# Optimization experiments

Measured on AMD Instinct MI355X. Metric: run time of the kernel, lower is better.

Reference implementation:

```python
import math
import jax, jax.numpy as jnp
import numpy as np

T, B, IN, H, D, ETA, R = 128, 32, 512, 8, 64, 4, 4
DE = ETA * D  # expanded key dim = eta * head_dim
EPS = 1e-05


def setup_inputs() -> dict:
    key = jax.random.key(0)
    ks = jax.random.split(key, 8)
    s = 0.05
    return {
        "inputs": jax.random.normal(ks[0], (T, B, IN), jnp.float32),
        "terminations": jnp.zeros((T, B), jnp.float32),
        "tilde_k_prev": jax.random.normal(ks[1], (B, R, H, DE), jnp.float32) * s,
        "tilde_v_prev": jax.random.normal(ks[2], (B, R, H, D), jnp.float32) * s,
        "s_prev": jax.random.normal(ks[3], (B, H, DE), jnp.float32) * s,
        "tick": jnp.zeros((B, 1), jnp.float32),
        "W_kqv": jax.random.normal(ks[4], (H * D * 5, IN), jnp.float32) * s,
        "b_kqv": jnp.zeros((H * D * 5,), jnp.float32),
        "W_p": jax.random.normal(ks[5], (H * ETA * 3, IN), jnp.float32) * s,
        "b_p": jnp.zeros((H * ETA * 3,), jnp.float32),
        "W_o": jax.random.normal(ks[6], (IN, H * D), jnp.float32) * s,
        "b_o": jnp.zeros((IN,), jnp.float32),
    }


def _forward(inputs, terminations, tilde_k_prev, tilde_v_prev, s_prev, tick,
             W_kqv, b_kqv, W_p, b_p, W_o, b_o):
    # projections
    kqv = (inputs @ W_kqv.T + b_kqv).reshape(T, B, H, 5, D)
    keys, queries, values, beta, gammas = (kqv[..., i, :] for i in range(5))
    p = (inputs @ W_p.T + b_p).reshape(T, B, H, 3, ETA)
    p1, p2, p3 = (p[..., i, :] for i in range(3))
    relu, sig = jax.nn.relu, jax.nn.sigmoid
    # kernel feature maps: outer product then flatten (d outer, n inner)
    keys = jnp.einsum('tbhd,tbhn->tbhdn', relu(keys), relu(p1)).reshape(T, B, H, DE)
    queries = jnp.einsum('tbhd,tbhn->tbhdn', relu(queries), relu(p2)).reshape(T, B, H, DE)
    gammas = jnp.einsum('tbhd,tbhn->tbhdn', sig(gammas), sig(p3)).reshape(T, B, H, DE)
    beta = sig(beta)  # (T,B,H,D)
    # oscillatory basis
    ticks = tick[None] + jnp.arange(1, T + 1, dtype=jnp.float32).reshape(T, 1, 1)  # (T,B,1)
    omegas = jnp.linspace(-math.pi, math.pi, R)
    occil = jnp.cos(ticks * omegas[None, None, :])  # (T,B,R)
    values = values * beta
    values_r = values[:, :, None] * occil[:, :, :, None, None]   # (T,B,R,H,D)
    keys_g = keys * gammas                                        # (T,B,H,DE)
    keys_r = keys_g[:, :, None] * occil[:, :, :, None, None]     # (T,B,R,H,DE)
    # discounts (with termination resets)
    nt = (1.0 - terminations)[:, :, None, None]
    dg = (1.0 - gammas) * nt  # (T,B,H,DE)
    db = (1.0 - beta) * nt    # (T,B,H,D)
    # recurrence y[t] = discount[t]*y[t-1] + x[t] via lax.scan over T
    def step(carry, xs):
        k_st, v_st, s_st = carry
        kx, vx, sx, dgt, dbt = xs
        k_new = dgt[:, None] * k_st + kx   # (B,R,H,DE)
        v_new = dbt[:, None] * v_st + vx   # (B,R,H,D)
        s_new = dgt * s_st + sx            # (B,H,DE)
        return (k_new, v_new, s_new), (k_new, v_new, s_new)
    (kf, vf, sf), (K, V, S) = jax.lax.scan(
        step, (tilde_k_prev, tilde_v_prev, s_prev), (keys_r, values_r, keys_g, dg, db))
    # attention readout
    kdq = jnp.einsum('tbrhd,tbhd->tbrh', K, queries)
    kv = jnp.einsum('tbrhd,tbrh->tbhd', V, kdq)
    norm = jnp.einsum('tbhd,tbhd->tbh', S, queries)
    attn = kv / (2 * R * norm[..., None] + EPS)  # (T,B,H,D)
    out = attn.reshape(T, B, H * D) @ W_o.T + b_o  # dropout p=0 (eval)
    return out, kf, vf, sf, tick + T


def reference(inputs, terminations, tilde_k_prev, tilde_v_prev, s_prev, tick,
              W_kqv, b_kqv, W_p, b_p, W_o, b_o):
    return _forward(inputs, terminations, tilde_k_prev, tilde_v_prev, s_prev, tick,
                    W_kqv, b_kqv, W_p, b_p, W_o, b_o)
```

## Files before the change

kernel.cpp:

```cpp
#include <hip/hip_runtime.h>
#include <math.h>
#include <stdint.h>

constexpr int T_ = 128, B_ = 32, IN_ = 512, H_ = 8, D_ = 64, ETA_ = 4, R_ = 4;
constexpr int DE_ = ETA_ * D_;
constexpr float EPS_ = 1e-5f;
constexpr int M_   = T_ * B_;
constexpr int BH_  = B_ * H_;
constexpr int NC2  = 16;
constexpr int CH2  = T_ / NC2;

constexpr int NW = 2688;
constexpr int SPLITCOL = 1664;

typedef __attribute__((ext_vector_type(8))) short bf16x8;
typedef __attribute__((ext_vector_type(4))) float f32x4;

__device__ __forceinline__ float bf2f(unsigned short u) {
    return __builtin_bit_cast(float, ((unsigned)u) << 16);
}
__device__ __forceinline__ unsigned short f2bf(float f) {
    unsigned u = __builtin_bit_cast(unsigned, f);
    u = (u + 0x7fffu + ((u >> 16) & 1u)) >> 16;
    return (unsigned short)u;
}
__device__ __forceinline__ float fsigm(float x) {
    return __fdividef(1.f, 1.f + __expf(-x));
}

__global__ __launch_bounds__(256) void cast_splitA(
    const float* __restrict__ src, unsigned short* __restrict__ dst, int n4)
{
    int i = blockIdx.x * 256 + threadIdx.x;
    if (i >= n4) return;
    const int r = i >> 7;
    const int c = (i & 127) << 2;
    float4 x = *(const float4*)(src + (size_t)r * 512 + c);
    ushort4 hi = make_ushort4(f2bf(x.x), f2bf(x.y), f2bf(x.z), f2bf(x.w));
    ushort4 lo = make_ushort4(f2bf(x.x - bf2f(hi.x)), f2bf(x.y - bf2f(hi.y)),
                              f2bf(x.z - bf2f(hi.z)), f2bf(x.w - bf2f(hi.w)));
    unsigned short* dr = dst + (size_t)r * 1024 + c;
    *(ushort4*)dr = hi;
    *(ushort4*)(dr + 512) = lo;
}

__global__ __launch_bounds__(256) void build_w2_bias(
    const float* __restrict__ Wkqv, const float* __restrict__ Wp,
    const float* __restrict__ bkqv, const float* __restrict__ bp,
    unsigned short* __restrict__ W2, float* __restrict__ bias_perm)
{
    int i = blockIdx.x * 256 + threadIdx.x;
    if (i >= NW * 128) return;
    const int rr = i >> 7;
    const int c = (i & 127) << 2;

    bool zero = false;
    const float* srow = nullptr;
    float bv = 0.f;
    if (rr < 512) {
        const int h = rr >> 6, dd = rr & 63, s = h * 320 + dd;
        srow = Wkqv + (size_t)s * 512; bv = bkqv[s];
    } else if (rr < 1024) {
        const int q = rr - 512, h = q >> 6, dd = q & 63, s = h * 320 + 64 + dd;
        srow = Wkqv + (size_t)s * 512; bv = bkqv[s];
    } else if (rr < 1536) {
        const int q = rr - 1024, h = q >> 6, dd = q & 63, s = h * 320 + 256 + dd;
        srow = Wkqv + (size_t)s * 512; bv = bkqv[s];
    } else if (rr < 1632) {
        const int q = rr - 1536;
        srow = Wp + (size_t)q * 512; bv = bp[q];
    } else if (rr < 1664) {
        zero = true;
    } else if (rr < 2176) {
        const int q = rr - 1664, h = q >> 6, dd = q & 63, s = h * 320 + 128 + dd;
        srow = Wkqv + (size_t)s * 512; bv = bkqv[s];
    } else {
        const int q = rr - 2176, h = q >> 6, dd = q & 63, s = h * 320 + 192 + dd;
        srow = Wkqv + (size_t)s * 512; bv = bkqv[s];
    }

    float4 x = zero ? make_float4(0.f, 0.f, 0.f, 0.f) : *(const float4*)(srow + c);
    ushort4 hi = make_ushort4(f2bf(x.x), f2bf(x.y), f2bf(x.z), f2bf(x.w));
    ushort4 lo = make_ushort4(f2bf(x.x - bf2f(hi.x)), f2bf(x.y - bf2f(hi.y)),
                              f2bf(x.z - bf2f(hi.z)), f2bf(x.w - bf2f(hi.w)));
    unsigned short* dr = W2 + (size_t)rr * 1536 + c;
    *(ushort4*)dr = hi;
    *(ushort4*)(dr + 512) = lo;
    *(ushort4*)(dr + 1024) = hi;
    if (c == 0) bias_perm[rr] = zero ? 0.f : bv;
}

__global__ __launch_bounds__(256) void cast_f32_bf16(
    const float* __restrict__ src, unsigned short* __restrict__ dst, int n8)
{
    int i = blockIdx.x * 256 + threadIdx.x;
    if (i >= n8) return;
    const float4* s = (const float4*)src;
    float4 a = s[2 * i], b = s[2 * i + 1];
    *(ushort4*)(dst + 8 * i)     = make_ushort4(f2bf(a.x), f2bf(a.y), f2bf(a.z), f2bf(a.w));
    *(ushort4*)(dst + 8 * i + 4) = make_ushort4(f2bf(b.x), f2bf(b.y), f2bf(b.z), f2bf(b.w));
}

__device__ __forceinline__ void gl_lds16(const unsigned short* g, unsigned short* l) {
    __builtin_amdgcn_global_load_lds((const __attribute__((address_space(1))) void*)g,
                                     (__attribute__((address_space(3))) void*)l, 16, 0, 0);
}

template <int BM, int BN>
__global__ __launch_bounds__(256) void gemm_bf16(
    const unsigned short* __restrict__ A,
    const unsigned short* __restrict__ W,
    const float* __restrict__ bias,
    float* __restrict__ C,
    int N, int sA, int sW, int kBig, int kSmall, int splitcol)
{
    constexpr int WM = BM / 2, WN = BN / 2;
    constexpr int AM = WM / 16, AN = WN / 16;
    constexpr int NLA = BM / 64;
    constexpr int NLB = BN / 64;
    constexpr int NLD = NLA + NLB;

    int bx, by;
    {
        const int nwg = gridDim.x * gridDim.y;
        int lin = blockIdx.y * gridDim.x + blockIdx.x;
        lin = (lin & 7) * (nwg >> 3) + (lin >> 3);
        const int G = (gridDim.x % 7 == 0) ? 7 : gridDim.x;
        const int grpsz = gridDim.y * G;
        const int cg = lin / grpsz, rem = lin % grpsz;
        by = rem / G;
        bx = cg * G + rem % G;
    }
    const int bm = by * BM;
    const int bn = bx * BN;
    const int tid = threadIdx.x;
    const int lane = tid & 63;
    const int wid = tid >> 6;
    const int wr = wid >> 1;
    const int wc = wid & 1;

    __shared__ __align__(16) unsigned short As[3][BM * 32];
    __shared__ __align__(16) unsigned short Bs[3][BN * 32];

    const unsigned short* aRow = A + (size_t)(bm + (tid & (BM - 1))) * sA
                                   + (tid / BM) * 8;
    const unsigned short* bRow = W + (size_t)(bn + (tid & (BN - 1))) * sW
                                   + (tid / BN) * 8;

    const int fA = (((lane >> 4) * BM) + wr * WM + (lane & 15)) * 8;
    const int fB = (((lane >> 4) * BN) + wc * WN + (lane & 15)) * 8;

    f32x4 acc[AM][AN] = {};
    const int K = (bn < splitcol) ? kBig : kSmall;
    const int NKT = K >> 5;

    auto stage = [&](int buf, int k0) {
        const int koA = (k0 >= 512) ? k0 - 512 : k0;
#pragma unroll
        for (int i = 0; i < NLA; ++i)
            gl_lds16(aRow + koA + i * (256 / BM) * 8,
                     &As[buf][(i * 256 + wid * 64) * 8]);
#pragma unroll
        for (int i = 0; i < NLB; ++i)
            gl_lds16(bRow + k0 + i * (256 / BN) * 8,
                     &Bs[buf][(i * 256 + wid * 64) * 8]);
    };

    stage(0, 0);
    if (NKT > 1) stage(1, 32);

    for (int kt = 0; kt < NKT; ++kt) {
        const int cur = kt % 3;
        if (kt + 2 < NKT) {
            stage((kt + 2) % 3, (kt + 2) << 5);
            if constexpr (NLD == 4)      asm volatile("s_waitcnt vmcnt(8)\ns_barrier" ::: "memory");
            else if constexpr (NLD == 3) asm volatile("s_waitcnt vmcnt(6)\ns_barrier" ::: "memory");
            else                         asm volatile("s_waitcnt vmcnt(4)\ns_barrier" ::: "memory");
        } else if (kt + 2 == NKT) {
            if constexpr (NLD == 4)      asm volatile("s_waitcnt vmcnt(4)\ns_barrier" ::: "memory");
            else if constexpr (NLD == 3) asm volatile("s_waitcnt vmcnt(3)\ns_barrier" ::: "memory");
            else                         asm volatile("s_waitcnt vmcnt(2)\ns_barrier" ::: "memory");
        } else {
            asm volatile("s_waitcnt vmcnt(0)\ns_barrier" ::: "memory");
        }
        __builtin_amdgcn_sched_barrier(0);

        bf16x8 af[AM], bfr[AN];
#pragma unroll
        for (int m = 0; m < AM; ++m) af[m] = *(const bf16x8*)&As[cur][fA + m * 128];
#pragma unroll
        for (int n = 0; n < AN; ++n) bfr[n] = *(const bf16x8*)&Bs[cur][fB + n * 128];
#pragma unroll
        for (int m = 0; m < AM; ++m)
#pragma unroll
            for (int n = 0; n < AN; ++n)
                acc[m][n] = __builtin_amdgcn_mfma_f32_16x16x32_bf16(af[m], bfr[n], acc[m][n], 0, 0, 0);

        asm volatile("s_waitcnt lgkmcnt(0)\ns_barrier" ::: "memory");
    }

#pragma unroll
    for (int n = 0; n < AN; ++n) {
        const int col = bn + wc * WN + n * 16 + (lane & 15);
        const float bv = bias[col];
#pragma unroll
        for (int m = 0; m < AM; ++m) {
            const int row0 = bm + wr * WM + m * 16 + ((lane >> 4) << 2);
#pragma unroll
            for (int j = 0; j < 4; ++j)
                C[(size_t)(row0 + j) * N + col] = acc[m][n][j] + bv;
        }
    }
}

template <int CTRL, int RM>
__device__ __forceinline__ float dpp_radd(float x) {
    int t = __builtin_amdgcn_update_dpp(0, __builtin_bit_cast(int, x), CTRL, RM, 0xf, true);
    return x + __builtin_bit_cast(float, t);
}
__device__ __forceinline__ float wave_allsum(float x) {
    x = dpp_radd<0x111, 0xf>(x);
    x = dpp_radd<0x112, 0xf>(x);
    x = dpp_radd<0x114, 0xf>(x);
    x = dpp_radd<0x118, 0xf>(x);
    x = dpp_radd<0x142, 0xa>(x);
    x = dpp_radd<0x143, 0xc>(x);
    return __builtin_bit_cast(float, __builtin_amdgcn_readlane(__builtin_bit_cast(int, x), 63));
}

__device__ __forceinline__ void osc2(float tt, float& oc03, float& oc12) {
    oc03 = cosf(3.14159265358979323846f * tt);
    oc12 = cosf(1.04719755119659774615f * tt);
}

__global__ __launch_bounds__(1024) void scan_fused(
    const float* __restrict__ kqv, const float* __restrict__ term,
    const float* __restrict__ tick,
    const float* __restrict__ k_prev, const float* __restrict__ v_prev,
    const float* __restrict__ s_prev,
    unsigned short* __restrict__ attn,
    float* __restrict__ kf, float* __restrict__ vf, float* __restrict__ sf,
    float* __restrict__ tick_out)
{
    const int bh = blockIdx.x;
    const int b = bh >> 3, h = bh & 7;
    const int tid = threadIdx.x;
    const int w = tid >> 6;
    const int d = tid & 63;

    __shared__ float LK[NC2][4][DE_];
    __shared__ float LS[NC2][DE_];
    __shared__ float LV[NC2][4][D_];
    __shared__ float LDg[NC2][DE_];
    __shared__ float LDb[NC2][D_];

    const float tk = tick[b];

    float K0[4] = {}, K1[4] = {}, K2[4] = {}, K3[4] = {}, S[4] = {};
    float V0 = 0.f, V1 = 0.f, V2 = 0.f, V3 = 0.f;
    float Dgv[4] = {1.f, 1.f, 1.f, 1.f};
    float Dbv = 1.f;

    if (w == 0) {
        float4 k4;
        k4 = *(const float4*)&k_prev[((size_t)(b * 4 + 0) * 8 + h) * DE_ + 4 * d];
        K0[0] = k4.x; K0[1] = k4.y; K0[2] = k4.z; K0[3] = k4.w;
        k4 = *(const float4*)&k_prev[((size_t)(b * 4 + 1) * 8 + h) * DE_ + 4 * d];
        K1[0] = k4.x; K1[1] = k4.y; K1[2] = k4.z; K1[3] = k4.w;
        k4 = *(const float4*)&k_prev[((size_t)(b * 4 + 2) * 8 + h) * DE_ + 4 * d];
        K2[0] = k4.x; K2[1] = k4.y; K2[2] = k4.z; K2[3] = k4.w;
        k4 = *(const float4*)&k_prev[((size_t)(b * 4 + 3) * 8 + h) * DE_ + 4 * d];
        K3[0] = k4.x; K3[1] = k4.y; K3[2] = k4.z; K3[3] = k4.w;
        k4 = *(const float4*)&s_prev[((size_t)b * 8 + h) * DE_ + 4 * d];
        S[0] = k4.x; S[1] = k4.y; S[2] = k4.z; S[3] = k4.w;
        V0 = v_prev[((size_t)(b * 4 + 0) * 8 + h) * D_ + d];
        V1 = v_prev[((size_t)(b * 4 + 1) * 8 + h) * D_ + d];
        V2 = v_prev[((size_t)(b * 4 + 2) * 8 + h) * D_ + d];
        V3 = v_prev[((size_t)(b * 4 + 3) * 8 + h) * D_ + d];
    }

    for (int t = w * CH2; t < w * CH2 + CH2; ++t) {
        const float* row = kqv + ((size_t)t * B_ + b) * NW;
        const float c0 = row[h * 64 + d];
        const float c2 = row[1664 + h * 64 + d];
        const float c3 = row[2176 + h * 64 + d];
        const float c4 = row[1024 + h * 64 + d];
        const float* pr = row + 1536 + h * 12;
        const float4 p1 = *(const float4*)pr;
        const float4 p3 = *(const float4*)(pr + 8);
        const float nt = 1.f - term[(size_t)t * B_ + b];

        float oc03, oc12; osc2(tk + (float)(t + 1), oc03, oc12);
        const float sgam = fsigm(c4);
        const float rk = fmaxf(c0, 0.f);
        const float sbet = fsigm(c3);
        const float vb = c2 * sbet;
        const float dbv = (1.f - sbet) * nt;
        const float p1a[4] = {p1.x, p1.y, p1.z, p1.w};
        const float p3a[4] = {p3.x, p3.y, p3.z, p3.w};
#pragma unroll
        for (int n = 0; n < 4; ++n) {
            const float g  = sgam * fsigm(p3a[n]);
            const float kg = rk * fmaxf(p1a[n], 0.f) * g;
            const float dg = (1.f - g) * nt;
            S[n]  = fmaf(dg, S[n],  kg);
            K0[n] = fmaf(dg, K0[n], kg * oc03);
            K1[n] = fmaf(dg, K1[n], kg * oc12);
            K2[n] = fmaf(dg, K2[n], kg * oc12);
            K3[n] = fmaf(dg, K3[n], kg * oc03);
            Dgv[n] *= dg;
        }
        V0 = fmaf(dbv, V0, vb * oc03);
        V1 = fmaf(dbv, V1, vb * oc12);
        V2 = fmaf(dbv, V2, vb * oc12);
        V3 = fmaf(dbv, V3, vb * oc03);
        Dbv *= dbv;
    }

    *(float4*)&LK[w][0][4 * d] = make_float4(K0[0], K0[1], K0[2], K0[3]);
    *(float4*)&LK[w][1][4 * d] = make_float4(K1[0], K1[1], K1[2], K1[3]);
    *(float4*)&LK[w][2][4 * d] = make_float4(K2[0], K2[1], K2[2], K2[3]);
    *(float4*)&LK[w][3][4 * d] = make_float4(K3[0], K3[1], K3[2], K3[3]);
    *(float4*)&LS[w][4 * d]    = make_float4(S[0], S[1], S[2], S[3]);
    LV[w][0][d] = V0; LV[w][1][d] = V1; LV[w][2][d] = V2; LV[w][3][d] = V3;
    *(float4*)&LDg[w][4 * d]   = make_float4(Dgv[0], Dgv[1], Dgv[2], Dgv[3]);
    LDb[w][d] = Dbv;
    __syncthreads();

    if (tid < DE_) {
        const int de = tid;
        float c0 = LK[0][0][de], c1k = LK[0][1][de], c2k = LK[0][2][de],
              c3k = LK[0][3][de], cs = LS[0][de];
        for (int c = 1; c < NC2; ++c) {
            const float dg = LDg[c][de];
            float n0 = fmaf(dg, c0,  LK[c][0][de]); LK[c][0][de] = c0;  c0  = n0;
            float n1 = fmaf(dg, c1k, LK[c][1][de]); LK[c][1][de] = c1k; c1k = n1;
            float n2 = fmaf(dg, c2k, LK[c][2][de]); LK[c][2][de] = c2k; c2k = n2;
            float n3 = fmaf(dg, c3k, LK[c][3][de]); LK[c][3][de] = c3k; c3k = n3;
            float ns = fmaf(dg, cs,  LS[c][de]);    LS[c][de]    = cs;  cs  = ns;
        }
        kf[((size_t)(b * 4 + 0) * 8 + h) * DE_ + de] = c0;
        kf[((size_t)(b * 4 + 1) * 8 + h) * DE_ + de] = c1k;
        kf[((size_t)(b * 4 + 2) * 8 + h) * DE_ + de] = c2k;
        kf[((size_t)(b * 4 + 3) * 8 + h) * DE_ + de] = c3k;
        sf[((size_t)b * 8 + h) * DE_ + de] = cs;
    } else if (tid < DE_ + D_) {
        const int dd = tid - DE_;
        float v0 = LV[0][0][dd], v1 = LV[0][1][dd], v2 = LV[0][2][dd], v3 = LV[0][3][dd];
        for (int c = 1; c < NC2; ++c) {
            const float db = LDb[c][dd];
            float n0 = fmaf(db, v0, LV[c][0][dd]); LV[c][0][dd] = v0; v0 = n0;
            float n1 = fmaf(db, v1, LV[c][1][dd]); LV[c][1][dd] = v1; v1 = n1;
            float n2 = fmaf(db, v2, LV[c][2][dd]); LV[c][2][dd] = v2; v2 = n2;
            float n3 = fmaf(db, v3, LV[c][3][dd]); LV[c][3][dd] = v3; v3 = n3;
        }
        vf[((size_t)(b * 4 + 0) * 8 + h) * D_ + dd] = v0;
        vf[((size_t)(b * 4 + 1) * 8 + h) * D_ + dd] = v1;
        vf[((size_t)(b * 4 + 2) * 8 + h) * D_ + dd] = v2;
        vf[((size_t)(b * 4 + 3) * 8 + h) * D_ + dd] = v3;
    }
    if (h == 0 && tid == 0) tick_out[b] = tk + (float)T_;
    __syncthreads();

    if (w == 0) {
        float4 k4;
        k4 = *(const float4*)&k_prev[((size_t)(b * 4 + 0) * 8 + h) * DE_ + 4 * d];
        K0[0] = k4.x; K0[1] = k4.y; K0[2] = k4.z; K0[3] = k4.w;
        k4 = *(const float4*)&k_prev[((size_t)(b * 4 + 1) * 8 + h) * DE_ + 4 * d];
        K1[0] = k4.x; K1[1] = k4.y; K1[2] = k4.z; K1[3] = k4.w;
        k4 = *(const float4*)&k_prev[((size_t)(b * 4 + 2) * 8 + h) * DE_ + 4 * d];
        K2[0] = k4.x; K2[1] = k4.y; K2[2] = k4.z; K2[3] = k4.w;
        k4 = *(const float4*)&k_prev[((size_t)(b * 4 + 3) * 8 + h) * DE_ + 4 * d];
        K3[0] = k4.x; K3[1] = k4.y; K3[2] = k4.z; K3[3] = k4.w;
        k4 = *(const float4*)&s_prev[((size_t)b * 8 + h) * DE_ + 4 * d];
        S[0] = k4.x; S[1] = k4.y; S[2] = k4.z; S[3] = k4.w;
        V0 = v_prev[((size_t)(b * 4 + 0) * 8 + h) * D_ + d];
        V1 = v_prev[((size_t)(b * 4 + 1) * 8 + h) * D_ + d];
        V2 = v_prev[((size_t)(b * 4 + 2) * 8 + h) * D_ + d];
        V3 = v_prev[((size_t)(b * 4 + 3) * 8 + h) * D_ + d];
    } else {
        float4 k4;
        k4 = *(const float4*)&LK[w][0][4 * d];
        K0[0] = k4.x; K0[1] = k4.y; K0[2] = k4.z; K0[3] = k4.w;
        k4 = *(const float4*)&LK[w][1][4 * d];
        K1[0] = k4.x; K1[1] = k4.y; K1[2] = k4.z; K1[3] = k4.w;
        k4 = *(const float4*)&LK[w][2][4 * d];
        K2[0] = k4.x; K2[1] = k4.y; K2[2] = k4.z; K2[3] = k4.w;
        k4 = *(const float4*)&LK[w][3][4 * d];
        K3[0] = k4.x; K3[1] = k4.y; K3[2] = k4.z; K3[3] = k4.w;
        k4 = *(const float4*)&LS[w][4 * d];
        S[0] = k4.x; S[1] = k4.y; S[2] = k4.z; S[3] = k4.w;
        V0 = LV[w][0][d]; V1 = LV[w][1][d]; V2 = LV[w][2][d]; V3 = LV[w][3][d];
    }

    for (int t = w * CH2; t < w * CH2 + CH2; ++t) {
        const float* row = kqv + ((size_t)t * B_ + b) * NW;
        const float c0 = row[h * 64 + d];
        const float c1 = row[512 + h * 64 + d];
        const float c2 = row[1664 + h * 64 + d];
        const float c3 = row[2176 + h * 64 + d];
        const float c4 = row[1024 + h * 64 + d];
        const float* pr = row + 1536 + h * 12;
        const float4 p1 = *(const float4*)pr;
        const float4 p2 = *(const float4*)(pr + 4);
        const float4 p3 = *(const float4*)(pr + 8);
        const float nt = 1.f - term[(size_t)t * B_ + b];

        float oc03, oc12; osc2(tk + (float)(t + 1), oc03, oc12);
        const float sgam = fsigm(c4);
        const float rk = fmaxf(c0, 0.f);
        const float rq = fmaxf(c1, 0.f);
        const float sbet = fsigm(c3);
        const float vb = c2 * sbet;
        const float dbv = (1.f - sbet) * nt;
        const float p1a[4] = {p1.x, p1.y, p1.z, p1.w};
        const float p2a[4] = {p2.x, p2.y, p2.z, p2.w};
        const float p3a[4] = {p3.x, p3.y, p3.z, p3.w};

        float s0 = 0.f, s1 = 0.f, s2 = 0.f, s3 = 0.f, s4 = 0.f;
#pragma unroll
        for (int n = 0; n < 4; ++n) {
            const float g  = sgam * fsigm(p3a[n]);
            const float kg = rk * fmaxf(p1a[n], 0.f) * g;
            const float qe = rq * fmaxf(p2a[n], 0.f);
            const float dg = (1.f - g) * nt;
            S[n]  = fmaf(dg, S[n],  kg);
            K0[n] = fmaf(dg, K0[n], kg * oc03);
            K1[n] = fmaf(dg, K1[n], kg * oc12);
            K2[n] = fmaf(dg, K2[n], kg * oc12);
            K3[n] = fmaf(dg, K3[n], kg * oc03);
            s0 = fmaf(K0[n], qe, s0);
            s1 = fmaf(K1[n], qe, s1);
            s2 = fmaf(K2[n], qe, s2);
            s3 = fmaf(K3[n], qe, s3);
            s4 = fmaf(S[n],  qe, s4);
        }
        V0 = fmaf(dbv, V0, vb * oc03);
        V1 = fmaf(dbv, V1, vb * oc12);
        V2 = fmaf(dbv, V2, vb * oc12);
        V3 = fmaf(dbv, V3, vb * oc03);

        const float kdq0 = wave_allsum(s0);
        const float kdq1 = wave_allsum(s1);
        const float kdq2 = wave_allsum(s2);
        const float kdq3 = wave_allsum(s3);
        const float nrm  = wave_allsum(s4);

        const float kv = V0 * kdq0 + V1 * kdq1 + V2 * kdq2 + V3 * kdq3;
        attn[((size_t)t * B_ + b) * (H_ * D_) + h * D_ + d] =
            f2bf(__fdividef(kv, 2.f * (float)R_ * nrm + EPS_));
    }
}

extern "C" void kernel_launch(void* const* d_in, const int* in_sizes, int n_in,
                              void* d_out, int out_size, void* d_ws, size_t ws_size,
                              hipStream_t stream)
{
    const float* inputs = (const float*)d_in[0];
    const float* term   = (const float*)d_in[1];
    const float* k_prev = (const float*)d_in[2];
    const float* v_prev = (const float*)d_in[3];
    const float* s_prev = (const float*)d_in[4];
    const float* tick   = (const float*)d_in[5];
    const float* W_kqv  = (const float*)d_in[6];
    const float* b_kqv  = (const float*)d_in[7];
    const float* W_p    = (const float*)d_in[8];
    const float* b_p    = (const float*)d_in[9];
    const float* W_o    = (const float*)d_in[10];
    const float* b_o    = (const float*)d_in[11];

    float* out = (float*)d_out;
    float* kf  = out + (size_t)T_ * B_ * IN_;
    float* vf  = kf  + (size_t)B_ * R_ * H_ * DE_;
    float* sf  = vf  + (size_t)B_ * R_ * H_ * D_;
    float* tick_out = sf + (size_t)B_ * H_ * DE_;

    float* kqv_s = (float*)d_ws;
    unsigned short* attn_bf = (unsigned short*)(kqv_s + (size_t)M_ * NW);
    unsigned short* Wo_bf   = attn_bf + (size_t)M_ * IN_;
    unsigned short* A2      = Wo_bf + (size_t)IN_ * (H_ * D_);
    unsigned short* W2      = A2 + (size_t)M_ * 1024;
    float* bias_perm        = (float*)(W2 + (size_t)NW * 1536);

    {
        int n4 = M_ * 128;
        cast_splitA<<<(n4 + 255) / 256, 256, 0, stream>>>(inputs, A2, n4);
        n4 = NW * 128;
        build_w2_bias<<<(n4 + 255) / 256, 256, 0, stream>>>(W_kqv, W_p, b_kqv, b_p,
                                                            W2, bias_perm);
        int n8 = (IN_ * (H_ * D_)) / 8;
        cast_f32_bf16<<<(n8 + 255) / 256, 256, 0, stream>>>(W_o, Wo_bf, n8);
    }

    {
        dim3 grid(NW / 128, M_ / 128);
        gemm_bf16<128, 128><<<grid, 256, 0, stream>>>(A2, W2, bias_perm, kqv_s,
                                                      NW, 1024, 1536, 1536, 512, SPLITCOL);
    }

    scan_fused<<<BH_, 1024, 0, stream>>>(kqv_s, term, tick, k_prev, v_prev, s_prev,
                                         attn_bf, kf, vf, sf, tick_out);

    {
        dim3 grid(IN_ / 64, M_ / 64);
        gemm_bf16<64, 64><<<grid, 256, 0, stream>>>(attn_bf, Wo_bf, b_o, out,
                                                    IN_, 512, 512, 512, 512, 0);
    }
}
```

Measured before the change: 139.0 us.

## Use 256x256-tile 512-thread GEMM for input projection with padded column layout

```diff
diff --git a/kernel.cpp b/kernel.cpp
--- a/kernel.cpp
+++ b/kernel.cpp
@@ -10,8 +10,8 @@
 constexpr int NC2  = 16;
 constexpr int CH2  = T_ / NC2;
 
-constexpr int NW = 2688;
-constexpr int SPLITCOL = 1664;
+constexpr int NW = 2816;
+constexpr int SPLITCOL = 1792;
 
 typedef __attribute__((ext_vector_type(8))) short bf16x8;
 typedef __attribute__((ext_vector_type(4))) float f32x4;
@@ -69,13 +69,13 @@
     } else if (rr < 1632) {
         const int q = rr - 1536;
         srow = Wp + (size_t)q * 512; bv = bp[q];
-    } else if (rr < 1664) {
+    } else if (rr < 1792) {
         zero = true;
-    } else if (rr < 2176) {
-        const int q = rr - 1664, h = q >> 6, dd = q & 63, s = h * 320 + 128 + dd;
+    } else if (rr < 2304) {
+        const int q = rr - 1792, h = q >> 6, dd = q & 63, s = h * 320 + 128 + dd;
         srow = Wkqv + (size_t)s * 512; bv = bkqv[s];
     } else {
-        const int q = rr - 2176, h = q >> 6, dd = q & 63, s = h * 320 + 192 + dd;
+        const int q = rr - 2304, h = q >> 6, dd = q & 63, s = h * 320 + 192 + dd;
         srow = Wkqv + (size_t)s * 512; bv = bkqv[s];
     }
 
@@ -106,20 +106,13 @@
                                      (__attribute__((address_space(3))) void*)l, 16, 0, 0);
 }
 
-template <int BM, int BN>
-__global__ __launch_bounds__(256) void gemm_bf16(
+__global__ __launch_bounds__(512) void gemm_big(
     const unsigned short* __restrict__ A,
     const unsigned short* __restrict__ W,
     const float* __restrict__ bias,
     float* __restrict__ C,
     int N, int sA, int sW, int kBig, int kSmall, int splitcol)
 {
-    constexpr int WM = BM / 2, WN = BN / 2;
-    constexpr int AM = WM / 16, AN = WN / 16;
-    constexpr int NLA = BM / 64;
-    constexpr int NLB = BN / 64;
-    constexpr int NLD = NLA + NLB;
-
     int bx, by;
     {
         const int nwg = gridDim.x * gridDim.y;
@@ -131,6 +124,111 @@
         by = rem / G;
         bx = cg * G + rem % G;
     }
+    const int bm = by * 256;
+    const int bn = bx * 256;
+    const int tid = threadIdx.x;
+    const int lane = tid & 63;
+    const int wid = tid >> 6;
+    const int wr = wid >> 2;
+    const int wc = wid & 3;
+
+    __shared__ __align__(16) unsigned short As[2][256 * 64];
+    __shared__ __align__(16) unsigned short Bs[2][256 * 64];
+
+    const int srow = tid & 255;
+    const int skg  = tid >> 8;
+    const unsigned short* aRow = A + (size_t)(bm + srow) * sA + skg * 8;
+    const unsigned short* bRow = W + (size_t)(bn + srow) * sW + skg * 8;
+
+    const int fA = (wr * 128 + (lane & 15)) * 8;
+    const int fB = (wc * 64 + (lane & 15)) * 8;
+
+    f32x4 acc[8][4] = {};
+    const int K = (bn < splitcol) ? kBig : kSmall;
+    const int NKT = K >> 6;
+
+    auto stage = [&](int buf, int k0) {
+        const int koA = (k0 >= 512) ? k0 - 512 : k0;
+#pragma unroll
+        for (int i = 0; i < 4; ++i)
+            gl_lds16(aRow + koA + i * 16, &As[buf][(i * 512 + tid) * 8]);
+#pragma unroll
+        for (int i = 0; i < 4; ++i)
+            gl_lds16(bRow + k0 + i * 16, &Bs[buf][(i * 512 + tid) * 8]);
+    };
+
+    stage(0, 0);
+
+    for (int kt = 0; kt < NKT; ++kt) {
+        const int cur = kt & 1;
+        if (kt + 1 < NKT) {
+            stage(cur ^ 1, (kt + 1) << 6);
+            asm volatile("s_waitcnt vmcnt(8)\ns_barrier" ::: "memory");
+        } else {
+            asm volatile("s_waitcnt vmcnt(0)\ns_barrier" ::: "memory");
+        }
+        __builtin_amdgcn_sched_barrier(0);
+
+#pragma unroll
+        for (int kk = 0; kk < 2; ++kk) {
+            const int base = (kk * 4 + (lane >> 4)) * 2048;
+            bf16x8 af[8], bfr[4];
+#pragma unroll
+            for (int m = 0; m < 8; ++m)
+                af[m] = *(const bf16x8*)&As[cur][base + fA + m * 128];
+#pragma unroll
+            for (int n = 0; n < 4; ++n)
+                bfr[n] = *(const bf16x8*)&Bs[cur][base + fB + n * 128];
+            __builtin_amdgcn_s_setprio(1);
+#pragma unroll
+            for (int m = 0; m < 8; ++m)
+#pragma unroll
+                for (int n = 0; n < 4; ++n)
+                    acc[m][n] = __builtin_amdgcn_mfma_f32_16x16x32_bf16(af[m], bfr[n], acc[m][n], 0, 0, 0);
+            __builtin_amdgcn_s_setprio(0);
+        }
+        asm volatile("s_waitcnt lgkmcnt(0)\ns_barrier" ::: "memory");
+    }
+
+#pragma unroll
+    for (int n = 0; n < 4; ++n) {
+        const int col = bn + wc * 64 + n * 16 + (lane & 15);
+        const float bv = bias[col];
+#pragma unroll
+        for (int m = 0; m < 8; ++m) {
+            const int row0 = bm + wr * 128 + m * 16 + ((lane >> 4) << 2);
+#pragma unroll
+            for (int j = 0; j < 4; ++j)
+                C[(size_t)(row0 + j) * N + col] = acc[m][n][j] + bv;
+        }
+    }
+}
+
+template <int BM, int BN>
+__global__ __launch_bounds__(256) void gemm_bf16(
+    const unsigned short* __restrict__ A,
+    const unsigned short* __restrict__ W,
+    const float* __restrict__ bias,
+    float* __restrict__ C,
+    int N, int sA, int sW, int K)
+{
+    constexpr int WM = BM / 2, WN = BN / 2;
+    constexpr int AM = WM / 16, AN = WN / 16;
+    constexpr int NLA = BM / 64;
+    constexpr int NLB = BN / 64;
+    constexpr int NLD = NLA + NLB;
+
+    int bx, by;
+    {
+        const int nwg = gridDim.x * gridDim.y;
+        int lin = blockIdx.y * gridDim.x + blockIdx.x;
+        lin = (lin & 7) * (nwg >> 3) + (lin >> 3);
+        const int G = (gridDim.x % 7 == 0) ? 7 : gridDim.x;
+        const int grpsz = gridDim.y * G;
+        const int cg = lin / grpsz, rem = lin % grpsz;
+        by = rem / G;
+        bx = cg * G + rem % G;
+    }
     const int bm = by * BM;
     const int bn = bx * BN;
     const int tid = threadIdx.x;
@@ -151,14 +249,12 @@
     const int fB = (((lane >> 4) * BN) + wc * WN + (lane & 15)) * 8;
 
     f32x4 acc[AM][AN] = {};
-    const int K = (bn < splitcol) ? kBig : kSmall;
     const int NKT = K >> 5;
 
     auto stage = [&](int buf, int k0) {
-        const int koA = (k0 >= 512) ? k0 - 512 : k0;
 #pragma unroll
         for (int i = 0; i < NLA; ++i)
-            gl_lds16(aRow + koA + i * (256 / BM) * 8,
+            gl_lds16(aRow + k0 + i * (256 / BM) * 8,
                      &As[buf][(i * 256 + wid * 64) * 8]);
 #pragma unroll
         for (int i = 0; i < NLB; ++i)
@@ -282,8 +378,8 @@
     for (int t = w * CH2; t < w * CH2 + CH2; ++t) {
         const float* row = kqv + ((size_t)t * B_ + b) * NW;
         const float c0 = row[h * 64 + d];
-        const float c2 = row[1664 + h * 64 + d];
-        const float c3 = row[2176 + h * 64 + d];
+        const float c2 = row[1792 + h * 64 + d];
+        const float c3 = row[2304 + h * 64 + d];
         const float c4 = row[1024 + h * 64 + d];
         const float* pr = row + 1536 + h * 12;
         const float4 p1 = *(const float4*)pr;
@@ -397,8 +493,8 @@
         const float* row = kqv + ((size_t)t * B_ + b) * NW;
         const float c0 = row[h * 64 + d];
         const float c1 = row[512 + h * 64 + d];
-        const float c2 = row[1664 + h * 64 + d];
-        const float c3 = row[2176 + h * 64 + d];
+        const float c2 = row[1792 + h * 64 + d];
+        const float c3 = row[2304 + h * 64 + d];
         const float c4 = row[1024 + h * 64 + d];
         const float* pr = row + 1536 + h * 12;
         const float4 p1 = *(const float4*)pr;
@@ -493,9 +589,9 @@
     }
 
     {
-        dim3 grid(NW / 128, M_ / 128);
-        gemm_bf16<128, 128><<<grid, 256, 0, stream>>>(A2, W2, bias_perm, kqv_s,
-                                                      NW, 1024, 1536, 1536, 512, SPLITCOL);
+        dim3 grid(NW / 256, M_ / 256);
+        gemm_big<<<grid, 512, 0, stream>>>(A2, W2, bias_perm, kqv_s,
+                                           NW, 1024, 1536, 1536, 512, SPLITCOL);
     }
 
     scan_fused<<<BH_, 1024, 0, stream>>>(kqv_s, term, tick, k_prev, v_prev, s_prev,
@@ -504,6 +600,6 @@
     {
         dim3 grid(IN_ / 64, M_ / 64);
         gemm_bf16<64, 64><<<grid, 256, 0, stream>>>(attn_bf, Wo_bf, b_o, out,
-                                                    IN_, 512, 512, 512, 512, 0);
-    }
-}
+                                                    IN_, 512, 512, 512);
+    }
+}
```

Result: no change. 141.7 us (+1.9%).
